# Kernel tuning notes

Hardware: AMD Instinct MI355X
Metric: run time of the kernel (lower is better)

## Reference

```python
import jax, jax.numpy as jnp
import numpy as np

N_HEADS = 16
D_HEAD = 64
MAX_POS = 128

def setup_inputs() -> dict:
    key = jax.random.key(0)
    ks = jax.random.split(key, 9)
    B, L, D = 4, 1024, 1024
    s = 0.02
    return {
        'x': jax.random.normal(ks[0], (B, L, D), jnp.float32),
        'pad_mask': jnp.ones((B, L), jnp.float32),
        'Wq': jax.random.normal(ks[1], (D, D), jnp.float32) * s,
        'bq': jnp.zeros((D,), jnp.float32),
        'Wk': jax.random.normal(ks[2], (D, D), jnp.float32) * s,
        'bk': jnp.zeros((D,), jnp.float32),
        'Wv': jax.random.normal(ks[3], (D, D), jnp.float32) * s,
        'bv': jnp.zeros((D,), jnp.float32),
        'Wo': jax.random.normal(ks[4], (D, D), jnp.float32) * s,
        'bo': jnp.zeros((D,), jnp.float32),
        'posK': jax.random.normal(ks[5], (2 * MAX_POS + 1, D_HEAD), jnp.float32) * s,
        'posV': jax.random.normal(ks[6], (2 * MAX_POS + 1, D_HEAD), jnp.float32) * s,
    }

def reference(x, pad_mask, Wq, bq, Wk, bk, Wv, bv, Wo, bo, posK, posV):
    B, L, _ = x.shape
    H, d = N_HEADS, D_HEAD
    def proj(W, b):
        y = x @ W + b                      # [B, L, H*d]
        return y.reshape(B, L, H, d).transpose(0, 2, 1, 3)  # [B, H, L, d]
    Q = proj(Wq, bq)
    K = proj(Wk, bk)
    V = proj(Wv, bv)
    # relative position index, clamped to [-MAX_POS, MAX_POS], shifted to [0, 2*MAX_POS]
    idx = jnp.arange(L)
    pos_index = jnp.clip(idx[None, :] - idx[:, None], -MAX_POS, MAX_POS) + MAX_POS  # [L, L]
    pos_emb_K = posK[pos_index]            # [L, L, d]
    pos_emb_V = posV[pos_index]            # [L, L, d]
    S1 = jnp.einsum('bhqd,bhkd->bhqk', Q, K)
    S2 = jnp.einsum('bhqd,qkd->bhqk', Q, pos_emb_K)
    S = (S1 + S2) / np.sqrt(d).astype(np.float32)
    # NOTE: original multiplies scores by the pad mask (not additive -inf)
    S = S * pad_mask[:, None, None, :]
    A = jax.nn.softmax(S, axis=-1)
    O1 = jnp.einsum('bhqk,bhkd->bhqd', A, V)
    O2 = jnp.einsum('bhqk,qkd->bhqd', A, pos_emb_V)
    out = (O1 + O2).transpose(0, 2, 1, 3).reshape(B, L, H * d)
    return out @ Wo + bo
```

## Files before the change

kernel.cpp:

```cpp
#include <hip/hip_runtime.h>
#include <math.h>

#define L_SEQ 1024
#define NB 4
#define NH 16
#define DH 64
#define BH_TOT (NB * NH)
#define GQ_TOT (BH_TOT * L_SEQ)
#define NPOS 257
#define QP_STRIDE 260
#define LDK 72
#define LDQP 72
#define LDPV 264

typedef unsigned short ushort_t;
typedef __attribute__((ext_vector_type(8))) short bf16x8;
typedef __attribute__((ext_vector_type(4))) float f32x4;

__device__ inline ushort_t f2bf_rne(float x) {
    unsigned u = __float_as_uint(x);
    unsigned r = u + 0x7FFFu + ((u >> 16) & 1u);
    return (ushort_t)(r >> 16);
}
__device__ inline float bf2f(ushort_t h) {
    return __uint_as_float(((unsigned)h) << 16);
}
__device__ inline void split8(float4 a0, float4 a1, uint4* H, uint4* L) {
    float v[8] = {a0.x, a0.y, a0.z, a0.w, a1.x, a1.y, a1.z, a1.w};
    unsigned hh[4], ll[4];
    #pragma unroll
    for (int j = 0; j < 4; j++) {
        ushort_t h0 = f2bf_rne(v[2*j]),   h1 = f2bf_rne(v[2*j+1]);
        ushort_t l0 = f2bf_rne(v[2*j]   - bf2f(h0));
        ushort_t l1 = f2bf_rne(v[2*j+1] - bf2f(h1));
        hh[j] = (unsigned)h0 | ((unsigned)h1 << 16);
        ll[j] = (unsigned)l0 | ((unsigned)l1 << 16);
    }
    *H = (uint4){hh[0], hh[1], hh[2], hh[3]};
    *L = (uint4){ll[0], ll[1], ll[2], ll[3]};
}
__device__ inline uint4 pack8hi(float4 a0, float4 a1) {
    float v[8] = {a0.x, a0.y, a0.z, a0.w, a1.x, a1.y, a1.z, a1.w};
    unsigned hh[4];
    #pragma unroll
    for (int j = 0; j < 4; j++)
        hh[j] = (unsigned)f2bf_rne(v[2*j]) | ((unsigned)f2bf_rne(v[2*j+1]) << 16);
    return (uint4){hh[0], hh[1], hh[2], hh[3]};
}

__global__ __launch_bounds__(256)
void split_f32_hi(const float* __restrict__ A, ushort_t* __restrict__ hi)
{
    const size_t base = ((size_t)blockIdx.x * 256 + threadIdx.x) * 8;
    *(uint4*)(hi + base) =
        pack8hi(*(const float4*)(A + base), *(const float4*)(A + base + 4));
}

__global__ __launch_bounds__(256)
void split_transpose(const float* __restrict__ W, ushort_t* __restrict__ Thi,
                     ushort_t* __restrict__ Tlo, int Kdim, int Ndim)
{
    __shared__ float Ws[64][65];
    const int tid = threadIdx.x;
    const int k0 = blockIdx.x * 64;
    const int n0 = blockIdx.y * 64;
    const int r  = tid >> 4;
    const int c4 = (tid & 15) * 4;
    #pragma unroll
    for (int i = 0; i < 4; i++) {
        float4 v = *(const float4*)(W + (size_t)(k0 + r + i*16) * Ndim + n0 + c4);
        Ws[r + i*16][c4+0] = v.x;
        Ws[r + i*16][c4+1] = v.y;
        Ws[r + i*16][c4+2] = v.z;
        Ws[r + i*16][c4+3] = v.w;
    }
    __syncthreads();
    #pragma unroll
    for (int i = 0; i < 4; i++) {
        const int nl = r + i*16;
        ushort_t h[4], l[4];
        #pragma unroll
        for (int j = 0; j < 4; j++) {
            float x = Ws[c4 + j][nl];
            h[j] = f2bf_rne(x);
            l[j] = f2bf_rne(x - bf2f(h[j]));
        }
        size_t off = (size_t)(n0 + nl) * Kdim + k0 + c4;
        uint2 H, L;
        H.x = (unsigned)h[0] | ((unsigned)h[1] << 16);
        H.y = (unsigned)h[2] | ((unsigned)h[3] << 16);
        L.x = (unsigned)l[0] | ((unsigned)l[1] << 16);
        L.y = (unsigned)l[2] | ((unsigned)l[3] << 16);
        *(uint2*)(Thi + off) = H;
        *(uint2*)(Tlo + off) = L;
    }
}

__global__ __launch_bounds__(256)
void prep_pvt(const float* __restrict__ posV, ushort_t* __restrict__ pvTg)
{
    __shared__ float Ws[64][65];
    const int tid = threadIdx.x;
    const int c = blockIdx.x;
    {
        const int r  = tid >> 2;
        const int d0 = (tid & 3) * 16;
        const float* src = posV + (size_t)(c * 64 + r + 1) * 64 + d0;
        #pragma unroll
        for (int i = 0; i < 4; i++) {
            float4 v = *(const float4*)(src + i * 4);
            Ws[r][d0 + i*4 + 0] = v.x;
            Ws[r][d0 + i*4 + 1] = v.y;
            Ws[r][d0 + i*4 + 2] = v.z;
            Ws[r][d0 + i*4 + 3] = v.w;
        }
    }
    __syncthreads();
    {
        const int d  = tid >> 2;
        const int r0 = (tid & 3) * 16;
        #pragma unroll
        for (int k = 0; k < 16; k++)
            pvTg[(size_t)d * LDPV + c * 64 + r0 + k] = f2bf_rne(Ws[r0 + k][d]);
    }
}

__global__ __launch_bounds__(256)
void gemm_mfma(const ushort_t* __restrict__ Ahi, const ushort_t* __restrict__ Alo,
               const ushort_t* __restrict__ Bhi, const ushort_t* __restrict__ Blo,
               const float* __restrict__ bias, void* __restrict__ Cout,
               int M, int N, int K, int mode, int nterms)
{
    __shared__ ushort_t As[2][64 * LDK];
    __shared__ ushort_t Bs[2][64 * LDK];
    const int tid  = threadIdx.x;
    const int m0   = blockIdx.x * 64;
    const int n0   = blockIdx.y * 64;
    const int wave = tid >> 6;
    const int lane = tid & 63;
    const int w0 = wave >> 1;
    const int w1 = wave & 1;
    const int lr = lane & 15;
    const int lq = lane >> 4;

    f32x4 acc[2][2];
    #pragma unroll
    for (int i = 0; i < 2; i++)
        #pragma unroll
        for (int j = 0; j < 2; j++)
            acc[i][j] = (f32x4){0.f, 0.f, 0.f, 0.f};

    for (int k0 = 0; k0 < K; k0 += 64) {
        __syncthreads();
        #pragma unroll
        for (int c = 0; c < 2; c++) {
            const int n   = c * 256 + tid;
            const int row = n >> 3;
            const int col = (n & 7) * 8;
            const size_t ga = (size_t)(m0 + row) * K + k0 + col;
            const size_t gb = (size_t)(n0 + row) * K + k0 + col;
            const int la = row * LDK + col;
            *(uint4*)&As[0][la] = *(const uint4*)(Ahi + ga);
            if (nterms == 3)
                *(uint4*)&As[1][la] = *(const uint4*)(Alo + ga);
            *(uint4*)&Bs[0][la] = *(const uint4*)(Bhi + gb);
            *(uint4*)&Bs[1][la] = *(const uint4*)(Blo + gb);
        }
        __syncthreads();
        #pragma unroll
        for (int ks = 0; ks < 2; ks++) {
            bf16x8 ah[2], bh[2], bl[2];
            #pragma unroll
            for (int i = 0; i < 2; i++) {
                const int ar = (w0*32 + i*16 + lr) * LDK + ks*32 + lq*8;
                ah[i] = *(const bf16x8*)&As[0][ar];
                const int br = (w1*32 + i*16 + lr) * LDK + ks*32 + lq*8;
                bh[i] = *(const bf16x8*)&Bs[0][br];
                bl[i] = *(const bf16x8*)&Bs[1][br];
            }
            #pragma unroll
            for (int i = 0; i < 2; i++)
                #pragma unroll
                for (int j = 0; j < 2; j++) {
                    acc[i][j] = __builtin_amdgcn_mfma_f32_16x16x32_bf16(ah[i], bh[j], acc[i][j], 0, 0, 0);
                    acc[i][j] = __builtin_amdgcn_mfma_f32_16x16x32_bf16(ah[i], bl[j], acc[i][j], 0, 0, 0);
                }
            if (nterms == 3) {
                bf16x8 al[2];
                #pragma unroll
                for (int i = 0; i < 2; i++)
                    al[i] = *(const bf16x8*)&As[1][(w0*32 + i*16 + lr) * LDK + ks*32 + lq*8];
                #pragma unroll
                for (int i = 0; i < 2; i++)
                    #pragma unroll
                    for (int j = 0; j < 2; j++)
                        acc[i][j] = __builtin_amdgcn_mfma_f32_16x16x32_bf16(al[i], bh[j], acc[i][j], 0, 0, 0);
            }
        }
    }

    #pragma unroll
    for (int j = 0; j < 2; j++) {
        const int colg = n0 + w1*32 + j*16 + lr;
        const float bcol = bias[colg];
        #pragma unroll
        for (int i = 0; i < 2; i++) {
            #pragma unroll
            for (int r = 0; r < 4; r++) {
                const int m = m0 + w0*32 + i*16 + lq*4 + r;
                const float v = acc[i][j][r] + bcol;
                if (mode == 0) {
                    ((float*)Cout)[(size_t)m * N + colg] = v;
                } else if (mode == 1) {
                    const int b = m >> 10, lp = m & 1023;
                    const int h = colg >> 6, dd = colg & 63;
                    ((float*)Cout)[((size_t)(b * NH + h) * L_SEQ + lp) * DH + dd] = v;
                } else if (mode == 2) {
                    const int b = m >> 10, lp = m & 1023;
                    const int h = colg >> 6, dd = colg & 63;
                    ((ushort_t*)Cout)[((size_t)(b * NH + h) * L_SEQ + lp) * DH + dd] = f2bf_rne(v);
                } else {
                    const int b = m >> 10, lp = m & 1023;
                    const int h = colg >> 6, dd = colg & 63;
                    ((ushort_t*)Cout)[((size_t)(b * NH + h) * DH + dd) * L_SEQ + lp] = f2bf_rne(v);
                }
            }
        }
    }
}

__global__ __launch_bounds__(256)
void qp_kernel(const float* __restrict__ Q, const float* __restrict__ posK,
               ushort_t* __restrict__ Qpu)
{
    __shared__ float Qt[64 * 64];
    __shared__ float Pt[64 * 64];
    const int tid = threadIdx.x;
    const size_t gq0 = (size_t)blockIdx.x * 64;
    const int ty = tid >> 4;
    const int tx = tid & 15;

    {
        const int q  = tid >> 2;
        const int d0 = (tid & 3) * 16;
        const float* qrow = Q + (gq0 + q) * DH + d0;
        #pragma unroll
        for (int i = 0; i < 4; i++) {
            float4 v = *(const float4*)(qrow + i * 4);
            Qt[(d0 + i*4 + 0) * 64 + q] = v.x;
            Qt[(d0 + i*4 + 1) * 64 + q] = v.y;
            Qt[(d0 + i*4 + 2) * 64 + q] = v.z;
            Qt[(d0 + i*4 + 3) * 64 + q] = v.w;
        }
    }

    for (int c = 0; c < 4; c++) {
        __syncthreads();
        {
            const int r  = tid >> 2;
            const int d0 = (tid & 3) * 16;
            const float* krow = posK + (size_t)(c * 64 + r) * DH + d0;
            #pragma unroll
            for (int i = 0; i < 4; i++) {
                float4 v = *(const float4*)(krow + i * 4);
                Pt[(d0 + i*4 + 0) * 64 + r] = v.x;
                Pt[(d0 + i*4 + 1) * 64 + r] = v.y;
                Pt[(d0 + i*4 + 2) * 64 + r] = v.z;
                Pt[(d0 + i*4 + 3) * 64 + r] = v.w;
            }
        }
        __syncthreads();

        float acc[16];
        #pragma unroll
        for (int i = 0; i < 16; i++) acc[i] = 0.f;
        #pragma unroll 16
        for (int d = 0; d < 64; d++) {
            float4 qv = *(const float4*)&Qt[d * 64 + ty * 4];
            float4 pv = *(const float4*)&Pt[d * 64 + tx * 4];
            float qa[4] = {qv.x, qv.y, qv.z, qv.w};
            float pa[4] = {pv.x, pv.y, pv.z, pv.w};
            #pragma unroll
            for (int i = 0; i < 4; i++)
                #pragma unroll
                for (int j = 0; j < 4; j++)
                    acc[i * 4 + j] += qa[i] * pa[j];
        }
        #pragma unroll
        for (int i = 0; i < 4; i++) {
            uint2 o;
            o.x = (unsigned)f2bf_rne(acc[i*4+0]) | ((unsigned)f2bf_rne(acc[i*4+1]) << 16);
            o.y = (unsigned)f2bf_rne(acc[i*4+2]) | ((unsigned)f2bf_rne(acc[i*4+3]) << 16);
            *(uint2*)(Qpu + (gq0 + ty * 4 + i) * QP_STRIDE + c * 64 + tx * 4) = o;
        }
    }

    __syncthreads();
    if (tid < 64) {
        float s = 0.f;
        #pragma unroll 16
        for (int d = 0; d < 64; d++)
            s += Qt[d * 64 + tid] * posK[256 * 64 + d];
        Qpu[(gq0 + tid) * QP_STRIDE + 256] = f2bf_rne(s);
    }
}

__global__ __launch_bounds__(256)
void attn_kernel(const float* __restrict__ Q, const ushort_t* __restrict__ Ku,
                 const ushort_t* __restrict__ Vtu, const ushort_t* __restrict__ Qpu,
                 const float* __restrict__ pm,
                 ushort_t* __restrict__ SbandU,
                 float* __restrict__ O1a, float* __restrict__ O1b,
                 float* __restrict__ lsum2, float* __restrict__ clo2,
                 float* __restrict__ chi2)
{
    __shared__ ushort_t Ks[64 * LDK];
    __shared__ ushort_t Vs[64 * LDK];
    __shared__ ushort_t QpsP[64 * LDQP];
    __shared__ float mk[64];

    const int tid = threadIdx.x;
    const int blk = blockIdx.x;
    const int bh  = blk >> 5;
    const int qb  = (blk >> 1) & 15;
    const int ks  = blk & 1;
    const int b   = bh >> 4;
    const int q0  = qb * 64;
    const size_t gq0 = (size_t)bh * L_SEQ + q0;
    const int wave = tid >> 6, lane = tid & 63;
    const int lr = lane & 15, lq = lane >> 4;
    const int qw = wave * 16;

    const int sr0 = tid >> 3,          sc0 = (tid & 7) * 8;
    const int sr1 = (256 + tid) >> 3,  sc1 = ((256 + tid) & 7) * 8;
    const int qpRowL = qw + (lane >> 2);
    const int qpCol0 = (lane & 3) * 16;

    const ushort_t* Kg  = Ku  + (size_t)bh * (L_SEQ * DH);
    const ushort_t* Vtg = Vtu + (size_t)bh * (DH * L_SEQ);

    bf16x8 qa[2];
    {
        const float* qrow = Q + (gq0 + qw + lr) * DH;
        #pragma unroll
        for (int kc = 0; kc < 2; kc++) {
            const float* s = qrow + kc * 32 + lq * 8;
            uint4 u = pack8hi(*(const float4*)s, *(const float4*)(s + 4));
            qa[kc] = *(bf16x8*)&u;
        }
    }

    if (ks == 0 && tid < 64) {
        const int q = q0 + tid;
        ushort_t* bandRow = SbandU + (gq0 + tid) * 256;
        for (int j = 0; j < 127 - q; j++)    bandRow[j] = 0;
        for (int j = 254; j > 1150 - q; j--) bandRow[j] = 0;
        bandRow[255] = 0;
    }

    f32x4 Oacc[4];
    #pragma unroll
    for (int j = 0; j < 4; j++) Oacc[j] = (f32x4){0.f, 0.f, 0.f, 0.f};
    float lpart[4] = {}, clpart[4] = {}, chpart[4] = {};

    uint4 kva0, kva1, kvb0, kvb1;
    ushort_t qpr[16];
    float mkr = 0.f;
    {
        const int k0 = ks * 512;
        kva0 = *(const uint4*)(Kg + (size_t)(k0 + sr0) * DH + sc0);
        kva1 = *(const uint4*)(Kg + (size_t)(k0 + sr1) * DH + sc1);
        kvb0 = *(const uint4*)(Vtg + (size_t)sr0 * L_SEQ + k0 + sc0);
        kvb1 = *(const uint4*)(Vtg + (size_t)sr1 * L_SEQ + k0 + sc1);
        const int qg = q0 + qpRowL;
        #pragma unroll
        for (int c = 0; c < 16; c++) {
            int rel = k0 + qpCol0 + c - qg;
            rel = rel < -128 ? -128 : (rel > 128 ? 128 : rel);
            qpr[c] = Qpu[(gq0 + qpRowL) * QP_STRIDE + rel + 128];
        }
        if (tid < 64) mkr = pm[b * L_SEQ + k0 + tid];
    }

    for (int t = 0; t < 8; t++) {
        const int k0 = (ks * 8 + t) * 64;
        __syncthreads();

        *(uint4*)&Ks[sr0 * LDK + sc0] = kva0;
        *(uint4*)&Ks[sr1 * LDK + sc1] = kva1;
        *(uint4*)&Vs[sr0 * LDK + sc0] = kvb0;
        *(uint4*)&Vs[sr1 * LDK + sc1] = kvb1;
        {
            ushort_t* dst = &QpsP[qpRowL * LDQP + qpCol0];
            #pragma unroll
            for (int c = 0; c < 8; c++)
                ((unsigned*)dst)[c] = (unsigned)qpr[2*c] | ((unsigned)qpr[2*c+1] << 16);
        }
        if (tid < 64) mk[tid] = mkr;
        __syncthreads();

        if (t < 7) {
            const int k0n = k0 + 64;
            kva0 = *(const uint4*)(Kg + (size_t)(k0n + sr0) * DH + sc0);
            kva1 = *(const uint4*)(Kg + (size_t)(k0n + sr1) * DH + sc1);
            kvb0 = *(const uint4*)(Vtg + (size_t)sr0 * L_SEQ + k0n + sc0);
            kvb1 = *(const uint4*)(Vtg + (size_t)sr1 * L_SEQ + k0n + sc1);
            const int qg = q0 + qpRowL;
            #pragma unroll
            for (int c = 0; c < 16; c++) {
                int rel = k0n + qpCol0 + c - qg;
                rel = rel < -128 ? -128 : (rel > 128 ? 128 : rel);
                qpr[c] = Qpu[(gq0 + qpRowL) * QP_STRIDE + rel + 128];
            }
            if (tid < 64) mkr = pm[b * L_SEQ + k0n + tid];
        }

        f32x4 Sacc[4];
        #pragma unroll
        for (int j = 0; j < 4; j++) Sacc[j] = (f32x4){0.f, 0.f, 0.f, 0.f};
        #pragma unroll
        for (int kc = 0; kc < 2; kc++) {
            #pragma unroll
            for (int j = 0; j < 4; j++) {
                bf16x8 kb = *(const bf16x8*)&Ks[(j*16 + lr) * LDK + kc*32 + lq*8];
                Sacc[j] = __builtin_amdgcn_mfma_f32_16x16x32_bf16(qa[kc], kb, Sacc[j], 0, 0, 0);
            }
        }

        ushort_t pb[4][4];
        #pragma unroll
        for (int r = 0; r < 4; r++) {
            const int ql = qw + lq*4 + r;
            const int q  = q0 + ql;
            const size_t gq = gq0 + ql;
            ushort_t* bandRow = SbandU + gq * 256 + 127;
            #pragma unroll
            for (int j = 0; j < 4; j++) {
                const int kl = j*16 + lr;
                const int k  = k0 + kl;
                const int rel = k - q;
                float s = (Sacc[j][r] + bf2f(QpsP[ql * LDQP + kl])) * 0.125f;
                s *= mk[kl];
                const float p = __expf(s);
                lpart[r] += p;
                const ushort_t ph = f2bf_rne(p);
                if (rel <= -128)      clpart[r] += p;
                else if (rel >= 128)  chpart[r] += p;
                else                  bandRow[rel] = ph;
                pb[j][r] = ph;
            }
        }

        #pragma unroll
        for (int r = 0; r < 4; r++)
            #pragma unroll
            for (int j = 0; j < 4; j++)
                QpsP[(qw + lq*4 + r) * LDQP + j*16 + lr] = pb[j][r];

        #pragma unroll
        for (int kc = 0; kc < 2; kc++) {
            bf16x8 pa = *(const bf16x8*)&QpsP[(qw + lr) * LDQP + kc*32 + lq*8];
            #pragma unroll
            for (int j = 0; j < 4; j++) {
                bf16x8 vb = *(const bf16x8*)&Vs[(j*16 + lr) * LDK + kc*32 + lq*8];
                Oacc[j] = __builtin_amdgcn_mfma_f32_16x16x32_bf16(pa, vb, Oacc[j], 0, 0, 0);
            }
        }
    }

    #pragma unroll
    for (int off = 1; off < 16; off <<= 1) {
        #pragma unroll
        for (int r = 0; r < 4; r++) {
            lpart[r]  += __shfl_xor(lpart[r],  off, 64);
            clpart[r] += __shfl_xor(clpart[r], off, 64);
            chpart[r] += __shfl_xor(chpart[r], off, 64);
        }
    }
    if (lr == 0) {
        #pragma unroll
        for (int r = 0; r < 4; r++) {
            const size_t o = (size_t)ks * GQ_TOT + gq0 + qw + lq*4 + r;
            lsum2[o] = lpart[r];
            clo2[o]  = clpart[r];
            chi2[o]  = chpart[r];
        }
    }

    float* O1o = ks ? O1b : O1a;
    #pragma unroll
    for (int j = 0; j < 4; j++)
        #pragma unroll
        for (int r = 0; r < 4; r++)
            O1o[(gq0 + qw + lq*4 + r) * DH + j*16 + lr] = Oacc[j][r];
}

__global__ __launch_bounds__(256)
void post_mfma(const ushort_t* __restrict__ SbandU, const ushort_t* __restrict__ pvTg,
               const float* __restrict__ O1a, const float* __restrict__ O1b,
               const float* __restrict__ lsum2, const float* __restrict__ clo2,
               const float* __restrict__ chi2, const float* __restrict__ posV,
               ushort_t* __restrict__ athi, ushort_t* __restrict__ atlo)
{
    __shared__ ushort_t pvT[64 * LDPV];
    const int tid = threadIdx.x;
    const size_t q0 = (size_t)blockIdx.x * 64;
    const int wave = tid >> 6, lane = tid & 63;
    const int w0 = wave >> 1, w1 = wave & 1;
    const int lr = lane & 15, lq = lane >> 4;

    {
        const unsigned* src = (const unsigned*)pvTg;
        unsigned* dst = (unsigned*)pvT;
        for (int i = tid; i < 64 * LDPV / 2; i += 256) dst[i] = src[i];
    }
    __syncthreads();

    f32x4 acc[2][2];
    #pragma unroll
    for (int i = 0; i < 2; i++)
        #pragma unroll
        for (int j = 0; j < 2; j++)
            acc[i][j] = (f32x4){0.f, 0.f, 0.f, 0.f};

    const ushort_t* bandB = SbandU + q0 * 256;
    #pragma unroll
    for (int kc = 0; kc < 8; kc++) {
        bf16x8 a[2], bv[2];
        #pragma unroll
        for (int i = 0; i < 2; i++) {
            a[i]  = *(const bf16x8*)&bandB[(size_t)(w0*32 + i*16 + lr) * 256 + kc*32 + lq*8];
            bv[i] = *(const bf16x8*)&pvT[(w1*32 + i*16 + lr) * LDPV + kc*32 + lq*8];
        }
        #pragma unroll
        for (int i = 0; i < 2; i++)
            #pragma unroll
            for (int j = 0; j < 2; j++)
                acc[i][j] = __builtin_amdgcn_mfma_f32_16x16x32_bf16(a[i], bv[j], acc[i][j], 0, 0, 0);
    }

    #pragma unroll
    for (int i = 0; i < 2; i++) {
        #pragma unroll
        for (int r = 0; r < 4; r++) {
            const int ql = w0*32 + i*16 + lq*4 + r;
            const size_t gq = q0 + ql;
            const float li = lsum2[gq] + lsum2[GQ_TOT + gq];
            const float cl = clo2[gq]  + clo2[GQ_TOT + gq];
            const float ch = chi2[gq]  + chi2[GQ_TOT + gq];
            const float inv = 1.0f / li;
            const int b  = (int)(gq >> 14);
            const int h  = (int)((gq >> 10) & 15);
            const int lp = (int)(gq & 1023);
            const size_t obase = ((size_t)(b * L_SEQ + lp) * 1024) + h * 64;
            #pragma unroll
            for (int j = 0; j < 2; j++) {
                const int dd = w1*32 + j*16 + lr;
                float o = O1a[gq * DH + dd] + O1b[gq * DH + dd] + acc[i][j][r]
                        + cl * posV[dd] + ch * posV[256 * 64 + dd];
                o *= inv;
                const ushort_t hh = f2bf_rne(o);
                const ushort_t ll = f2bf_rne(o - bf2f(hh));
                athi[obase + dd] = hh;
                atlo[obase + dd] = ll;
            }
        }
    }
}

extern "C" void kernel_launch(void* const* d_in, const int* in_sizes, int n_in,
                              void* d_out, int out_size, void* d_ws, size_t ws_size,
                              hipStream_t stream)
{
    const float* x    = (const float*)d_in[0];
    const float* pmk  = (const float*)d_in[1];
    const float* Wq   = (const float*)d_in[2];
    const float* bq   = (const float*)d_in[3];
    const float* Wk   = (const float*)d_in[4];
    const float* bk   = (const float*)d_in[5];
    const float* Wv   = (const float*)d_in[6];
    const float* bv   = (const float*)d_in[7];
    const float* Wo   = (const float*)d_in[8];
    const float* bo   = (const float*)d_in[9];
    const float* posK = (const float*)d_in[10];
    const float* posV = (const float*)d_in[11];
    float* out = (float*)d_out;

    float* ws = (float*)d_ws;
    float* Qb = ws;
    ushort_t* Kbu = (ushort_t*)(Qb + (size_t)GQ_TOT * DH);
    ushort_t* Vtu = Kbu + (size_t)GQ_TOT * DH;
    ushort_t* Qpu = Vtu + (size_t)GQ_TOT * DH;
    ushort_t* SbandU = Qpu + (size_t)GQ_TOT * QP_STRIDE;
    ushort_t* athi = SbandU + (size_t)GQ_TOT * 256;
    ushort_t* atlo = athi + (size_t)GQ_TOT * DH;
    ushort_t* pvTg = atlo + (size_t)GQ_TOT * DH;
    float* O1a   = (float*)(pvTg + 64 * LDPV);
    float* O1b   = O1a   + (size_t)GQ_TOT * DH;
    float* lsum2 = O1b   + (size_t)GQ_TOT * DH;
    float* clo2  = lsum2 + 2 * (size_t)GQ_TOT;
    float* chi2  = clo2  + 2 * (size_t)GQ_TOT;

    ushort_t* bb  = SbandU;
    ushort_t* xhi = bb;
    ushort_t* wqh = xhi + 4194304;
    ushort_t* wql = wqh + 1048576;
    ushort_t* wkh = wql + 1048576;
    ushort_t* wkl = wkh + 1048576;
    ushort_t* wvh = wkl + 1048576;
    ushort_t* wvl = wvh + 1048576;
    ushort_t* woh = bb;
    ushort_t* wol = woh + 1048576;

    dim3 tg(16, 16), gg(64, 16), gb(256);

    split_f32_hi<<<dim3(2048), gb, 0, stream>>>(x, xhi);
    split_transpose<<<tg, gb, 0, stream>>>(Wq, wqh, wql, 1024, 1024);
    split_transpose<<<tg, gb, 0, stream>>>(Wk, wkh, wkl, 1024, 1024);
    split_transpose<<<tg, gb, 0, stream>>>(Wv, wvh, wvl, 1024, 1024);
    prep_pvt<<<dim3(4), gb, 0, stream>>>(posV, pvTg);
    gemm_mfma<<<gg, gb, 0, stream>>>(xhi, xhi, wqh, wql, bq, Qb,  4096, 1024, 1024, 1, 2);
    gemm_mfma<<<gg, gb, 0, stream>>>(xhi, xhi, wkh, wkl, bk, Kbu, 4096, 1024, 1024, 2, 2);
    gemm_mfma<<<gg, gb, 0, stream>>>(xhi, xhi, wvh, wvl, bv, Vtu, 4096, 1024, 1024, 3, 2);
    qp_kernel<<<dim3(GQ_TOT / 64), gb, 0, stream>>>(Qb, posK, Qpu);
    attn_kernel<<<dim3(2048), gb, 0, stream>>>(Qb, Kbu, Vtu, Qpu, pmk,
                                               SbandU, O1a, O1b, lsum2, clo2, chi2);
    post_mfma<<<dim3(GQ_TOT / 64), gb, 0, stream>>>(SbandU, pvTg, O1a, O1b, lsum2,
                                                    clo2, chi2, posV, athi, atlo);
    split_transpose<<<tg, gb, 0, stream>>>(Wo, woh, wol, 1024, 1024);
    gemm_mfma<<<gg, gb, 0, stream>>>(athi, atlo, woh, wol, bo, out, 4096, 1024, 1024, 0, 3);
}
```

Before: 419.4 us.

## Fuse QKV projections into one GEMM and move Q·posK to MFMA

The three weight split-transposes are merged into one 3D-grid launch, and the three Q/K/V GEMMs become a single gemm_qkv launch with 3x the N tiles that picks its bias and output layout per tile. The scalar-FP32 qp_kernel is replaced by qp_mfma, which converts Q and posK to bf16 in registers and uses MFMA. The generic gemm_mfma loses its runtime mode and nterms branches and keeps only the 3-term path for the output projection. This is meant to cut launch overhead, give one larger grid, and remove the FP32 FMA cost of the Q·posK product. In exchange, qp_mfma rounds Q to bf16, and its grid of 5 column tiles rereads Q per tile and wastes most of the last one.

```diff
diff --git a/kernel.cpp b/kernel.cpp
--- a/kernel.cpp
+++ b/kernel.cpp
@@ -57,6 +57,51 @@
 }
 
 __global__ __launch_bounds__(256)
+void split_transpose3(const float* __restrict__ Wq, const float* __restrict__ Wk,
+                      const float* __restrict__ Wv, ushort_t* __restrict__ Thi,
+                      ushort_t* __restrict__ Tlo)
+{
+    __shared__ float Ws[64][65];
+    const int tid = threadIdx.x;
+    const int k0 = blockIdx.x * 64;
+    const int n0 = blockIdx.y * 64;
+    const int z  = blockIdx.z;
+    const float* W = (z == 0) ? Wq : (z == 1) ? Wk : Wv;
+    ushort_t* Hh = Thi + (size_t)z * 1048576;
+    ushort_t* Ll = Tlo + (size_t)z * 1048576;
+    const int r  = tid >> 4;
+    const int c4 = (tid & 15) * 4;
+    #pragma unroll
+    for (int i = 0; i < 4; i++) {
+        float4 v = *(const float4*)(W + (size_t)(k0 + r + i*16) * 1024 + n0 + c4);
+        Ws[r + i*16][c4+0] = v.x;
+        Ws[r + i*16][c4+1] = v.y;
+        Ws[r + i*16][c4+2] = v.z;
+        Ws[r + i*16][c4+3] = v.w;
+    }
+    __syncthreads();
+    #pragma unroll
+    for (int i = 0; i < 4; i++) {
+        const int nl = r + i*16;
+        ushort_t h[4], l[4];
+        #pragma unroll
+        for (int j = 0; j < 4; j++) {
+            float x = Ws[c4 + j][nl];
+            h[j] = f2bf_rne(x);
+            l[j] = f2bf_rne(x - bf2f(h[j]));
+        }
+        size_t off = (size_t)(n0 + nl) * 1024 + k0 + c4;
+        uint2 H, L;
+        H.x = (unsigned)h[0] | ((unsigned)h[1] << 16);
+        H.y = (unsigned)h[2] | ((unsigned)h[3] << 16);
+        L.x = (unsigned)l[0] | ((unsigned)l[1] << 16);
+        L.y = (unsigned)l[2] | ((unsigned)l[3] << 16);
+        *(uint2*)(Hh + off) = H;
+        *(uint2*)(Ll + off) = L;
+    }
+}
+
+__global__ __launch_bounds__(256)
 void split_transpose(const float* __restrict__ W, ushort_t* __restrict__ Thi,
                      ushort_t* __restrict__ Tlo, int Kdim, int Ndim)
 {
@@ -126,22 +171,106 @@
 }
 
 __global__ __launch_bounds__(256)
+void gemm_qkv(const ushort_t* __restrict__ Ahi,
+              const ushort_t* __restrict__ Bhi, const ushort_t* __restrict__ Blo,
+              const float* __restrict__ bq, const float* __restrict__ bk,
+              const float* __restrict__ bv,
+              float* __restrict__ Qb, ushort_t* __restrict__ Kbu,
+              ushort_t* __restrict__ Vtu)
+{
+    __shared__ ushort_t As[64 * LDK];
+    __shared__ ushort_t Bs[2][64 * LDK];
+    const int tid  = threadIdx.x;
+    const int m0   = blockIdx.x * 64;
+    const int n0   = blockIdx.y * 64;
+    const int nb   = n0 >> 10;
+    const int wave = tid >> 6, lane = tid & 63;
+    const int w0 = wave >> 1, w1 = wave & 1;
+    const int lr = lane & 15, lq = lane >> 4;
+    const int K = 1024;
+
+    f32x4 acc[2][2];
+    #pragma unroll
+    for (int i = 0; i < 2; i++)
+        #pragma unroll
+        for (int j = 0; j < 2; j++)
+            acc[i][j] = (f32x4){0.f, 0.f, 0.f, 0.f};
+
+    for (int k0 = 0; k0 < K; k0 += 64) {
+        __syncthreads();
+        #pragma unroll
+        for (int c = 0; c < 2; c++) {
+            const int n   = c * 256 + tid;
+            const int row = n >> 3;
+            const int col = (n & 7) * 8;
+            const size_t ga = (size_t)(m0 + row) * K + k0 + col;
+            const size_t gb = (size_t)(n0 + row) * K + k0 + col;
+            const int la = row * LDK + col;
+            *(uint4*)&As[la]    = *(const uint4*)(Ahi + ga);
+            *(uint4*)&Bs[0][la] = *(const uint4*)(Bhi + gb);
+            *(uint4*)&Bs[1][la] = *(const uint4*)(Blo + gb);
+        }
+        __syncthreads();
+        #pragma unroll
+        for (int ks = 0; ks < 2; ks++) {
+            bf16x8 ah[2], bh[2], bl[2];
+            #pragma unroll
+            for (int i = 0; i < 2; i++) {
+                const int ar = (w0*32 + i*16 + lr) * LDK + ks*32 + lq*8;
+                ah[i] = *(const bf16x8*)&As[ar];
+                const int br = (w1*32 + i*16 + lr) * LDK + ks*32 + lq*8;
+                bh[i] = *(const bf16x8*)&Bs[0][br];
+                bl[i] = *(const bf16x8*)&Bs[1][br];
+            }
+            #pragma unroll
+            for (int i = 0; i < 2; i++)
+                #pragma unroll
+                for (int j = 0; j < 2; j++) {
+                    acc[i][j] = __builtin_amdgcn_mfma_f32_16x16x32_bf16(ah[i], bh[j], acc[i][j], 0, 0, 0);
+                    acc[i][j] = __builtin_amdgcn_mfma_f32_16x16x32_bf16(ah[i], bl[j], acc[i][j], 0, 0, 0);
+                }
+        }
+    }
+
+    const float* bp = (nb == 0) ? bq : (nb == 1) ? bk : bv;
+    #pragma unroll
+    for (int j = 0; j < 2; j++) {
+        const int colg = n0 + w1*32 + j*16 + lr;
+        const int c1   = colg & 1023;
+        const float bcol = bp[c1];
+        const int h = c1 >> 6, dd = c1 & 63;
+        #pragma unroll
+        for (int i = 0; i < 2; i++) {
+            #pragma unroll
+            for (int r = 0; r < 4; r++) {
+                const int m = m0 + w0*32 + i*16 + lq*4 + r;
+                const float v = acc[i][j][r] + bcol;
+                const int b = m >> 10, lp = m & 1023;
+                if (nb == 0)
+                    Qb[((size_t)(b * NH + h) * L_SEQ + lp) * DH + dd] = v;
+                else if (nb == 1)
+                    Kbu[((size_t)(b * NH + h) * L_SEQ + lp) * DH + dd] = f2bf_rne(v);
+                else
+                    Vtu[((size_t)(b * NH + h) * DH + dd) * L_SEQ + lp] = f2bf_rne(v);
+            }
+        }
+    }
+}
+
+__global__ __launch_bounds__(256)
 void gemm_mfma(const ushort_t* __restrict__ Ahi, const ushort_t* __restrict__ Alo,
                const ushort_t* __restrict__ Bhi, const ushort_t* __restrict__ Blo,
-               const float* __restrict__ bias, void* __restrict__ Cout,
-               int M, int N, int K, int mode, int nterms)
+               const float* __restrict__ bias, float* __restrict__ C,
+               int M, int N, int K)
 {
     __shared__ ushort_t As[2][64 * LDK];
     __shared__ ushort_t Bs[2][64 * LDK];
     const int tid  = threadIdx.x;
     const int m0   = blockIdx.x * 64;
     const int n0   = blockIdx.y * 64;
-    const int wave = tid >> 6;
-    const int lane = tid & 63;
-    const int w0 = wave >> 1;
-    const int w1 = wave & 1;
-    const int lr = lane & 15;
-    const int lq = lane >> 4;
+    const int wave = tid >> 6, lane = tid & 63;
+    const int w0 = wave >> 1, w1 = wave & 1;
+    const int lr = lane & 15, lq = lane >> 4;
 
     f32x4 acc[2][2];
     #pragma unroll
@@ -161,19 +290,19 @@
             const size_t gb = (size_t)(n0 + row) * K + k0 + col;
             const int la = row * LDK + col;
             *(uint4*)&As[0][la] = *(const uint4*)(Ahi + ga);
-            if (nterms == 3)
-                *(uint4*)&As[1][la] = *(const uint4*)(Alo + ga);
+            *(uint4*)&As[1][la] = *(const uint4*)(Alo + ga);
             *(uint4*)&Bs[0][la] = *(const uint4*)(Bhi + gb);
             *(uint4*)&Bs[1][la] = *(const uint4*)(Blo + gb);
         }
         __syncthreads();
         #pragma unroll
         for (int ks = 0; ks < 2; ks++) {
-            bf16x8 ah[2], bh[2], bl[2];
+            bf16x8 ah[2], al[2], bh[2], bl[2];
             #pragma unroll
             for (int i = 0; i < 2; i++) {
                 const int ar = (w0*32 + i*16 + lr) * LDK + ks*32 + lq*8;
                 ah[i] = *(const bf16x8*)&As[0][ar];
+                al[i] = *(const bf16x8*)&As[1][ar];
                 const int br = (w1*32 + i*16 + lr) * LDK + ks*32 + lq*8;
                 bh[i] = *(const bf16x8*)&Bs[0][br];
                 bl[i] = *(const bf16x8*)&Bs[1][br];
@@ -184,18 +313,8 @@
                 for (int j = 0; j < 2; j++) {
                     acc[i][j] = __builtin_amdgcn_mfma_f32_16x16x32_bf16(ah[i], bh[j], acc[i][j], 0, 0, 0);
                     acc[i][j] = __builtin_amdgcn_mfma_f32_16x16x32_bf16(ah[i], bl[j], acc[i][j], 0, 0, 0);
+                    acc[i][j] = __builtin_amdgcn_mfma_f32_16x16x32_bf16(al[i], bh[j], acc[i][j], 0, 0, 0);
                 }
-            if (nterms == 3) {
-                bf16x8 al[2];
-                #pragma unroll
-                for (int i = 0; i < 2; i++)
-                    al[i] = *(const bf16x8*)&As[1][(w0*32 + i*16 + lr) * LDK + ks*32 + lq*8];
-                #pragma unroll
-                for (int i = 0; i < 2; i++)
-                    #pragma unroll
-                    for (int j = 0; j < 2; j++)
-                        acc[i][j] = __builtin_amdgcn_mfma_f32_16x16x32_bf16(al[i], bh[j], acc[i][j], 0, 0, 0);
-            }
         }
     }
 
@@ -208,101 +327,74 @@
             #pragma unroll
             for (int r = 0; r < 4; r++) {
                 const int m = m0 + w0*32 + i*16 + lq*4 + r;
-                const float v = acc[i][j][r] + bcol;
-                if (mode == 0) {
-                    ((float*)Cout)[(size_t)m * N + colg] = v;
-                } else if (mode == 1) {
-                    const int b = m >> 10, lp = m & 1023;
-                    const int h = colg >> 6, dd = colg & 63;
-                    ((float*)Cout)[((size_t)(b * NH + h) * L_SEQ + lp) * DH + dd] = v;
-                } else if (mode == 2) {
-                    const int b = m >> 10, lp = m & 1023;
-                    const int h = colg >> 6, dd = colg & 63;
-                    ((ushort_t*)Cout)[((size_t)(b * NH + h) * L_SEQ + lp) * DH + dd] = f2bf_rne(v);
-                } else {
-                    const int b = m >> 10, lp = m & 1023;
-                    const int h = colg >> 6, dd = colg & 63;
-                    ((ushort_t*)Cout)[((size_t)(b * NH + h) * DH + dd) * L_SEQ + lp] = f2bf_rne(v);
+                C[(size_t)m * N + colg] = acc[i][j][r] + bcol;
+            }
+        }
+    }
+}
+
+__global__ __launch_bounds__(256)
+void qp_mfma(const float* __restrict__ Q, const float* __restrict__ posK,
+             ushort_t* __restrict__ Qpu)
+{
+    const int tid = threadIdx.x;
+    const size_t m0 = (size_t)blockIdx.x * 64;
+    const int n0 = blockIdx.y * 64;
+    const int wave = tid >> 6, lane = tid & 63;
+    const int wm = (wave >> 1) * 32, wn = (wave & 1) * 32;
+    const int lr = lane & 15, lq = lane >> 4;
+
+    bf16x8 af[2][2];
+    #pragma unroll
+    for (int i = 0; i < 2; i++) {
+        const float* qrow = Q + (m0 + wm + i*16 + lr) * DH;
+        #pragma unroll
+        for (int kc = 0; kc < 2; kc++) {
+            const float* s = qrow + kc*32 + lq*8;
+            uint4 u = pack8hi(*(const float4*)s, *(const float4*)(s + 4));
+            af[i][kc] = *(bf16x8*)&u;
+        }
+    }
+    bf16x8 bf[2][2];
+    #pragma unroll
+    for (int j = 0; j < 2; j++) {
+        int n = n0 + wn + j*16 + lr;
+        const float* krow = posK + (size_t)(n < 256 ? n : 256) * DH;
+        #pragma unroll
+        for (int kc = 0; kc < 2; kc++) {
+            const float* s = krow + kc*32 + lq*8;
+            uint4 u = pack8hi(*(const float4*)s, *(const float4*)(s + 4));
+            bf[j][kc] = *(bf16x8*)&u;
+        }
+    }
+
+    f32x4 acc[2][2];
+    #pragma unroll
+    for (int i = 0; i < 2; i++)
+        #pragma unroll
+        for (int j = 0; j < 2; j++)
+            acc[i][j] = (f32x4){0.f, 0.f, 0.f, 0.f};
+    #pragma unroll
+    for (int kc = 0; kc < 2; kc++)
+        #pragma unroll
+        for (int i = 0; i < 2; i++)
+            #pragma unroll
+            for (int j = 0; j < 2; j++)
+                acc[i][j] = __builtin_amdgcn_mfma_f32_16x16x32_bf16(af[i][kc], bf[j][kc], acc[i][j], 0, 0, 0);
+
+    #pragma unroll
+    for (int i = 0; i < 2; i++)
+        #pragma unroll
+        for (int j = 0; j < 2; j++) {
+            const int n = n0 + wn + j*16 + lr;
+            if (n < NPOS) {
+                #pragma unroll
+                for (int r = 0; r < 4; r++) {
+                    const size_t m = m0 + wm + i*16 + lq*4 + r;
+                    Qpu[m * QP_STRIDE + n] = f2bf_rne(acc[i][j][r]);
                 }
             }
         }
-    }
-}
-
-__global__ __launch_bounds__(256)
-void qp_kernel(const float* __restrict__ Q, const float* __restrict__ posK,
-               ushort_t* __restrict__ Qpu)
-{
-    __shared__ float Qt[64 * 64];
-    __shared__ float Pt[64 * 64];
-    const int tid = threadIdx.x;
-    const size_t gq0 = (size_t)blockIdx.x * 64;
-    const int ty = tid >> 4;
-    const int tx = tid & 15;
-
-    {
-        const int q  = tid >> 2;
-        const int d0 = (tid & 3) * 16;
-        const float* qrow = Q + (gq0 + q) * DH + d0;
-        #pragma unroll
-        for (int i = 0; i < 4; i++) {
-            float4 v = *(const float4*)(qrow + i * 4);
-            Qt[(d0 + i*4 + 0) * 64 + q] = v.x;
-            Qt[(d0 + i*4 + 1) * 64 + q] = v.y;
-            Qt[(d0 + i*4 + 2) * 64 + q] = v.z;
-            Qt[(d0 + i*4 + 3) * 64 + q] = v.w;
-        }
-    }
-
-    for (int c = 0; c < 4; c++) {
-        __syncthreads();
-        {
-            const int r  = tid >> 2;
-            const int d0 = (tid & 3) * 16;
-            const float* krow = posK + (size_t)(c * 64 + r) * DH + d0;
-            #pragma unroll
-            for (int i = 0; i < 4; i++) {
-                float4 v = *(const float4*)(krow + i * 4);
-                Pt[(d0 + i*4 + 0) * 64 + r] = v.x;
-                Pt[(d0 + i*4 + 1) * 64 + r] = v.y;
-                Pt[(d0 + i*4 + 2) * 64 + r] = v.z;
-                Pt[(d0 + i*4 + 3) * 64 + r] = v.w;
-            }
-        }
-        __syncthreads();
-
-        float acc[16];
-        #pragma unroll
-        for (int i = 0; i < 16; i++) acc[i] = 0.f;
-        #pragma unroll 16
-        for (int d = 0; d < 64; d++) {
-            float4 qv = *(const float4*)&Qt[d * 64 + ty * 4];
-            float4 pv = *(const float4*)&Pt[d * 64 + tx * 4];
-            float qa[4] = {qv.x, qv.y, qv.z, qv.w};
-            float pa[4] = {pv.x, pv.y, pv.z, pv.w};
-            #pragma unroll
-            for (int i = 0; i < 4; i++)
-                #pragma unroll
-                for (int j = 0; j < 4; j++)
-                    acc[i * 4 + j] += qa[i] * pa[j];
-        }
-        #pragma unroll
-        for (int i = 0; i < 4; i++) {
-            uint2 o;
-            o.x = (unsigned)f2bf_rne(acc[i*4+0]) | ((unsigned)f2bf_rne(acc[i*4+1]) << 16);
-            o.y = (unsigned)f2bf_rne(acc[i*4+2]) | ((unsigned)f2bf_rne(acc[i*4+3]) << 16);
-            *(uint2*)(Qpu + (gq0 + ty * 4 + i) * QP_STRIDE + c * 64 + tx * 4) = o;
-        }
-    }
-
-    __syncthreads();
-    if (tid < 64) {
-        float s = 0.f;
-        #pragma unroll 16
-        for (int d = 0; d < 64; d++)
-            s += Qt[d * 64 + tid] * posK[256 * 64 + d];
-        Qpu[(gq0 + tid) * QP_STRIDE + 256] = f2bf_rne(s);
-    }
 }
 
 __global__ __launch_bounds__(256)
@@ -601,32 +693,26 @@
     float* clo2  = lsum2 + 2 * (size_t)GQ_TOT;
     float* chi2  = clo2  + 2 * (size_t)GQ_TOT;
 
-    ushort_t* bb  = SbandU;
-    ushort_t* xhi = bb;
-    ushort_t* wqh = xhi + 4194304;
-    ushort_t* wql = wqh + 1048576;
-    ushort_t* wkh = wql + 1048576;
-    ushort_t* wkl = wkh + 1048576;
-    ushort_t* wvh = wkl + 1048576;
-    ushort_t* wvl = wvh + 1048576;
-    ushort_t* woh = bb;
-    ushort_t* wol = woh + 1048576;
-
-    dim3 tg(16, 16), gg(64, 16), gb(256);
+    ushort_t* bb    = SbandU;
+    ushort_t* xhi   = bb;
+    ushort_t* wqkvh = xhi + 4194304;
+    ushort_t* wqkvl = wqkvh + 3145728;
+    ushort_t* woh   = bb;
+    ushort_t* wol   = woh + 1048576;
+
+    dim3 gb(256);
 
     split_f32_hi<<<dim3(2048), gb, 0, stream>>>(x, xhi);
-    split_transpose<<<tg, gb, 0, stream>>>(Wq, wqh, wql, 1024, 1024);
-    split_transpose<<<tg, gb, 0, stream>>>(Wk, wkh, wkl, 1024, 1024);
-    split_transpose<<<tg, gb, 0, stream>>>(Wv, wvh, wvl, 1024, 1024);
+    split_transpose3<<<dim3(16, 16, 3), gb, 0, stream>>>(Wq, Wk, Wv, wqkvh, wqkvl);
     prep_pvt<<<dim3(4), gb, 0, stream>>>(posV, pvTg);
-    gemm_mfma<<<gg, gb, 0, stream>>>(xhi, xhi, wqh, wql, bq, Qb,  4096, 1024, 1024, 1, 2);
-    gemm_mfma<<<gg, gb, 0, stream>>>(xhi, xhi, wkh, wkl, bk, Kbu, 4096, 1024, 1024, 2, 2);
-    gemm_mfma<<<gg, gb, 0, stream>>>(xhi, xhi, wvh, wvl, bv, Vtu, 4096, 1024, 1024, 3, 2);
-    qp_kernel<<<dim3(GQ_TOT / 64), gb, 0, stream>>>(Qb, posK, Qpu);
+    gemm_qkv<<<dim3(64, 48), gb, 0, stream>>>(xhi, wqkvh, wqkvl, bq, bk, bv,
+                                              Qb, Kbu, Vtu);
+    qp_mfma<<<dim3(1024, 5), gb, 0, stream>>>(Qb, posK, Qpu);
     attn_kernel<<<dim3(2048), gb, 0, stream>>>(Qb, Kbu, Vtu, Qpu, pmk,
                                                SbandU, O1a, O1b, lsum2, clo2, chi2);
     post_mfma<<<dim3(GQ_TOT / 64), gb, 0, stream>>>(SbandU, pvTg, O1a, O1b, lsum2,
                                                     clo2, chi2, posV, athi, atlo);
-    split_transpose<<<tg, gb, 0, stream>>>(Wo, woh, wol, 1024, 1024);
-    gemm_mfma<<<gg, gb, 0, stream>>>(athi, atlo, woh, wol, bo, out, 4096, 1024, 1024, 0, 3);
-}
+    split_transpose<<<dim3(16, 16), gb, 0, stream>>>(Wo, woh, wol, 1024, 1024);
+    gemm_mfma<<<dim3(64, 16), gb, 0, stream>>>(athi, atlo, woh, wol, bo, out,
+                                               4096, 1024, 1024);
+}
```

After: 384.1 us. 1.09x faster.
